# Kernel tuning notes

Measured on AMD Instinct MI355X. Metric: run time of the kernel, lower is better.

Reference implementation:

```python
import jax, jax.numpy as jnp
import numpy as np

D_MODEL = 512
NUM_HEADS = 8
D_K = D_MODEL // NUM_HEADS


def setup_inputs() -> dict:
    key = jax.random.key(0)
    ks = jax.random.split(key, 13)
    B, S = 2, 4096
    s = 1.0 / np.sqrt(D_MODEL)
    inp = {
        'Q': jax.random.normal(ks[0], (B, S, D_MODEL), jnp.float32),
        'K': jax.random.normal(ks[1], (B, S, D_MODEL), jnp.float32),
        'V': jax.random.normal(ks[2], (B, S, D_MODEL), jnp.float32),
        'mask': jax.random.randint(ks[3], (B, S), 0, 2, jnp.int32),
        'W_q': jax.random.normal(ks[4], (D_MODEL, D_MODEL), jnp.float32) * s,
        'b_q': jnp.zeros((D_MODEL,), jnp.float32),
        'W_k': jax.random.normal(ks[5], (D_MODEL, D_MODEL), jnp.float32) * s,
        'b_k': jnp.zeros((D_MODEL,), jnp.float32),
        'W_v': jax.random.normal(ks[6], (D_MODEL, D_MODEL), jnp.float32) * s,
        'b_v': jnp.zeros((D_MODEL,), jnp.float32),
        'W_o': jax.random.normal(ks[7], (D_MODEL, D_MODEL), jnp.float32) * s,
        'b_o': jnp.zeros((D_MODEL,), jnp.float32),
    }
    return inp


def _split_heads(x):
    B, S, _ = x.shape
    return x.reshape(B, S, NUM_HEADS, D_K).transpose(0, 2, 1, 3)  # [B,H,S,d_k]


def reference(Q, K, V, mask, W_q, b_q, W_k, b_k, W_v, b_v, W_o, b_o):
    q = _split_heads(Q @ W_q.T + b_q)
    k = _split_heads(K @ W_k.T + b_k)
    v = _split_heads(V @ W_v.T + b_v)
    scores = jnp.einsum('bhqd,bhkd->bhqk', q, k) / jnp.sqrt(jnp.float32(D_K))
    # mask [B,S] broadcast over heads and query dim (key dim masked)
    scores = jnp.where(mask[:, None, None, :] == 0, jnp.float32(-1e9), scores)
    probs = jax.nn.softmax(scores, axis=-1)
    attn = jnp.einsum('bhqk,bhkd->bhqd', probs, v)
    B, H, S, dk = attn.shape
    combined = attn.transpose(0, 2, 1, 3).reshape(B, S, D_MODEL)
    return combined @ W_o.T + b_o
```

## Files before the change

kernel.cpp:

```cpp
#include <hip/hip_runtime.h>
#include <hip/hip_bf16.h>

typedef _Float16 h8 __attribute__((ext_vector_type(8)));
typedef _Float16 h4 __attribute__((ext_vector_type(4)));
typedef _Float16 h2 __attribute__((ext_vector_type(2)));
typedef float f2 __attribute__((ext_vector_type(2)));
typedef float f4 __attribute__((ext_vector_type(4)));
typedef float f16v __attribute__((ext_vector_type(16)));

#define MFMA32(a, b, c) __builtin_amdgcn_mfma_f32_32x32x16_f16(a, b, c, 0, 0, 0)

static constexpr int DM = 512;
static constexpr int SL = 4096;
static constexpr int NH = 8;
static constexpr int DK = 64;
static constexpr int NB = 2;

__device__ __forceinline__ h2 pk2(float a, float b) {
    return __builtin_bit_cast(h2, __builtin_amdgcn_cvt_pkrtz(a, b));
}
__device__ __forceinline__ h8 cvt8(float4 x, float4 y) {
    union { h2 h[4]; h8 v; } u;
    u.h[0] = pk2(x.x, x.y); u.h[1] = pk2(x.z, x.w);
    u.h[2] = pk2(y.x, y.y); u.h[3] = pk2(y.z, y.w);
    return u.v;
}

__global__ __launch_bounds__(256) void proj_qkv_kernel(
    const float* __restrict__ Qin, const float* __restrict__ Kin,
    const float* __restrict__ Vin,
    const float* __restrict__ Wq, const float* __restrict__ Wk,
    const float* __restrict__ Wv,
    const float* __restrict__ bq, const float* __restrict__ bk,
    const float* __restrict__ bv,
    _Float16* __restrict__ qo, _Float16* __restrict__ ko,
    _Float16* __restrict__ vTo)
{
    const int bid = blockIdx.x;
    const int op  = (bid & 7) * 96 + (bid >> 3);
    const int nt    = op & 3;
    const int panel = op >> 2;
    const int which = panel >> 6;
    const int mt    = panel & 63;

    const float* __restrict__ X    = which == 0 ? Qin : (which == 1 ? Kin : Vin);
    const float* __restrict__ W    = which == 0 ? Wq  : (which == 1 ? Wk  : Wv);
    const float* __restrict__ bias = which == 0 ? bq  : (which == 1 ? bk  : bv);

    __shared__ __align__(16) _Float16 As[2][4096];
    __shared__ __align__(16) _Float16 Bs[2][4096];
    __shared__ __align__(16) _Float16 Vtr[64][144];

    const int t   = threadIdx.x;
    const int w   = t >> 6;
    const int l   = t & 63;
    const int l31 = l & 31;
    const int hi  = l >> 5;
    const int mbase = mt * 128;
    const int nbase = nt * 128;
    const int wm = (w >> 1) * 64;
    const int wn = (w & 1) * 64;

    const int id0 = t, id1 = 256 + t;
    const int r0 = id0 >> 2, c0 = id0 & 3;
    const int r1 = id1 >> 2, c1 = id1 & 3;
    const int sl0 = (c0 ^ (r0 & 3)) * 8;
    const int sl1 = (c1 ^ (r1 & 3)) * 8;
    const float* Xp0 = X + (size_t)(mbase + r0) * DM + c0 * 8;
    const float* Xp1 = X + (size_t)(mbase + r1) * DM + c1 * 8;
    const float* Wp0 = W + (size_t)(nbase + r0) * DM + c0 * 8;
    const float* Wp1 = W + (size_t)(nbase + r1) * DM + c1 * 8;

    f16v acc[2][2] = {};

    {
        float4 a00 = *(const float4*)(Xp0), a01 = *(const float4*)(Xp0 + 4);
        float4 a10 = *(const float4*)(Xp1), a11 = *(const float4*)(Xp1 + 4);
        float4 b00 = *(const float4*)(Wp0), b01 = *(const float4*)(Wp0 + 4);
        float4 b10 = *(const float4*)(Wp1), b11 = *(const float4*)(Wp1 + 4);
        *(h8*)&As[0][r0 * 32 + sl0] = cvt8(a00, a01);
        *(h8*)&As[0][r1 * 32 + sl1] = cvt8(a10, a11);
        *(h8*)&Bs[0][r0 * 32 + sl0] = cvt8(b00, b01);
        *(h8*)&Bs[0][r1 * 32 + sl1] = cvt8(b10, b11);
    }
    __syncthreads();

    int cur = 0;
    for (int step = 0; step < 16; ++step) {
        const int kn = (step + 1) * 32;
        float4 a00, a01, a10, a11, b00, b01, b10, b11;
        const bool more = step + 1 < 16;
        if (more) {
            a00 = *(const float4*)(Xp0 + kn); a01 = *(const float4*)(Xp0 + kn + 4);
            a10 = *(const float4*)(Xp1 + kn); a11 = *(const float4*)(Xp1 + kn + 4);
            b00 = *(const float4*)(Wp0 + kn); b01 = *(const float4*)(Wp0 + kn + 4);
            b10 = *(const float4*)(Wp1 + kn); b11 = *(const float4*)(Wp1 + kn + 4);
        }

        const _Float16* Ac = As[cur];
        const _Float16* Bc = Bs[cur];
        h8 af[2][2], bf[2][2];
#pragma unroll
        for (int ti = 0; ti < 2; ++ti)
#pragma unroll
            for (int s = 0; s < 2; ++s)
                af[ti][s] = *(const h8*)&Ac[(wm + ti * 32 + l31) * 32 +
                                            (((2 * s + hi) ^ (l31 & 3)) << 3)];
#pragma unroll
        for (int tj = 0; tj < 2; ++tj)
#pragma unroll
            for (int s = 0; s < 2; ++s)
                bf[tj][s] = *(const h8*)&Bc[(wn + tj * 32 + l31) * 32 +
                                            (((2 * s + hi) ^ (l31 & 3)) << 3)];
        __builtin_amdgcn_s_setprio(1);
#pragma unroll
        for (int ti = 0; ti < 2; ++ti)
#pragma unroll
            for (int tj = 0; tj < 2; ++tj)
#pragma unroll
                for (int s = 0; s < 2; ++s)
                    acc[ti][tj] = MFMA32(af[ti][s], bf[tj][s], acc[ti][tj]);
        __builtin_amdgcn_s_setprio(0);

        if (more) {
            const int nb2 = cur ^ 1;
            *(h8*)&As[nb2][r0 * 32 + sl0] = cvt8(a00, a01);
            *(h8*)&As[nb2][r1 * 32 + sl1] = cvt8(a10, a11);
            *(h8*)&Bs[nb2][r0 * 32 + sl0] = cvt8(b00, b01);
            *(h8*)&Bs[nb2][r1 * 32 + sl1] = cvt8(b10, b11);
        }
        __syncthreads();
        cur ^= 1;
    }

    if (which < 2) {
        _Float16* dst = (which == 0) ? qo : ko;
#pragma unroll
        for (int tj = 0; tj < 2; ++tj) {
            const int n  = nbase + wn + tj * 32 + l31;
            const float bb = bias[n];
            const int hh = n >> 6;
            const int d  = n & 63;
#pragma unroll
            for (int ti = 0; ti < 2; ++ti) {
#pragma unroll
                for (int j = 0; j < 4; ++j) {
#pragma unroll
                    for (int c = 0; c < 4; ++c) {
                        const int m = mbase + wm + ti * 32 + 8 * j + 4 * hi + c;
                        const int bi = m >> 12;
                        const int s  = m & 4095;
                        dst[((size_t)(bi * NH + hh) * SL + s) * DK + d] =
                            (_Float16)(acc[ti][tj][4 * j + c] + bb);
                    }
                }
            }
        }
    } else {
        const int bi = mbase >> 12;
        const int s0 = mbase & 4095;
#pragma unroll
        for (int nh = 0; nh < 2; ++nh) {
            __syncthreads();
            if ((w & 1) == nh) {
#pragma unroll
                for (int tj = 0; tj < 2; ++tj) {
                    const int d = tj * 32 + l31;
                    const float bb = bias[nbase + nh * 64 + d];
#pragma unroll
                    for (int ti = 0; ti < 2; ++ti) {
#pragma unroll
                        for (int j = 0; j < 4; ++j) {
                            h2 x0 = pk2(acc[ti][tj][4 * j] + bb,
                                        acc[ti][tj][4 * j + 1] + bb);
                            h2 x1 = pk2(acc[ti][tj][4 * j + 2] + bb,
                                        acc[ti][tj][4 * j + 3] + bb);
                            h4 val = {x0[0], x0[1], x1[0], x1[1]};
                            *(h4*)&Vtr[d][wm + ti * 32 + 8 * j + 4 * hi] = val;
                        }
                    }
                }
            }
            __syncthreads();
            {
                const int d = t >> 2, part = t & 3;
                const int hh = nt * 2 + nh;
                _Float16* dstv = vTo + ((size_t)(bi * NH + hh) * DK + d) * SL +
                                 s0 + part * 32;
                h8 v0 = *(const h8*)&Vtr[d][part * 32];
                h8 v1 = *(const h8*)&Vtr[d][part * 32 + 8];
                h8 v2 = *(const h8*)&Vtr[d][part * 32 + 16];
                h8 v3 = *(const h8*)&Vtr[d][part * 32 + 24];
                *(h8*)(dstv)      = v0;
                *(h8*)(dstv + 8)  = v1;
                *(h8*)(dstv + 16) = v2;
                *(h8*)(dstv + 24) = v3;
            }
        }
    }
}

static constexpr int QBLK  = 256;
static constexpr int KSPL  = 2;
static constexpr int KHALF = SL / KSPL;
static constexpr int NTS   = KHALF / 64;

__device__ __forceinline__ void stage_tiles(
    _Float16* Ktb, _Float16* Vtb,
    const _Float16* kbh, const _Float16* vbh, int kb, int t)
{
    const int w = t >> 6;
    const char* ksrc = (const char*)(kbh + (size_t)kb * DK);
    {
        const int c  = t;
        const int kr = c >> 3;
        const int sl = c & 7;
        const int srow = (kr & ~12) | ((kr & 4) << 1) | ((kr & 8) >> 1);
        const int cs = srow * 8 + (sl ^ (kr & 7));
        char* dst = (char*)Ktb + (size_t)w * 1024;
        __builtin_amdgcn_global_load_lds(
            (const __attribute__((address_space(1))) void*)(ksrc + (size_t)cs * 16),
            (__attribute__((address_space(3))) void*)dst, 16, 0, 0);
    }
    {
        const int c  = t;
        const int d  = c >> 3;
        const int cs = (c & 7) ^ (d & 7);
        const _Float16* src = vbh + (size_t)d * SL + kb + cs * 8;
        char* dst = (char*)Vtb + (size_t)w * 1024;
        __builtin_amdgcn_global_load_lds(
            (const __attribute__((address_space(1))) void*)src,
            (__attribute__((address_space(3))) void*)dst, 16, 0, 0);
    }
}

__global__ __launch_bounds__(512, 4) void attn_kernel(
    const _Float16* __restrict__ qg, const _Float16* __restrict__ kg,
    const _Float16* __restrict__ vTg, const int* __restrict__ mask,
    _Float16* __restrict__ o_ws, float* __restrict__ l_ws)
{
    const int t   = threadIdx.x;
    const int w   = t >> 6;
    const int l   = t & 63;
    const int l31 = l & 31;
    const int hi  = l >> 5;
    const int r7  = l31 & 7;
    const int hh  = blockIdx.x & 7;
    const int b   = blockIdx.x >> 3;
    const int qt  = blockIdx.y;
    const int split = blockIdx.z;
    const int koff  = split * KHALF;

    const _Float16* qbh = qg  + (size_t)(b * NH + hh) * SL * DK;
    const _Float16* kbh = kg  + (size_t)(b * NH + hh) * SL * DK;
    const _Float16* vbh = vTg + (size_t)(b * NH + hh) * DK * SL;
    const int* mrow = mask + b * SL;

    __shared__ __align__(16) _Float16 Kt[2][4096];
    __shared__ __align__(16) _Float16 Vt[2][4096];
    __shared__ __align__(16) float bias_tab[KHALF];

    {
        int4 v = *(const int4*)&mrow[koff + t * 4];
        f4 bv;
        bv[0] = v.x ? 0.f : -1e38f; bv[1] = v.y ? 0.f : -1e38f;
        bv[2] = v.z ? 0.f : -1e38f; bv[3] = v.w ? 0.f : -1e38f;
        *(f4*)&bias_tab[t * 4] = bv;
    }

    const _Float16 sch = (_Float16)(0.125f * 1.44269504089f);
    const h8 sc8 = {sch, sch, sch, sch, sch, sch, sch, sch};
    h8 qf[4];
    {
        const _Float16* qp = qbh + (size_t)(qt * QBLK + w * 32 + l31) * DK + hi * 8;
#pragma unroll
        for (int st = 0; st < 4; ++st)
            qf[st] = *(const h8*)(qp + st * 16) * sc8;
    }

    stage_tiles(Kt[0], Vt[0], kbh, vbh, koff, t);
    __syncthreads();

    f16v ov[2] = {};
    float lsum = 0.f;
    const h2 one2 = {(_Float16)1.0f, (_Float16)1.0f};

    int cur = 0;
    for (int kt = 0; kt < NTS; ++kt) {
        const int kb = koff + kt * 64;
        if (kt + 1 < NTS)
            stage_tiles(Kt[cur ^ 1], Vt[cur ^ 1], kbh, vbh, kb + 64, t);

        const _Float16* Kc = Kt[cur];
        const _Float16* Vc = Vt[cur];
        const int lb = kt * 64;

        f16v sc[2];
#pragma unroll
        for (int s = 0; s < 2; ++s) {
            union { f2 q[8]; f16v v; } u;
#pragma unroll
            for (int j = 0; j < 4; ++j) {
                const int base = lb + s * 32 + ((j >> 1) << 4) +
                                 ((j & 1) << 2) + (hi << 3);
                u.q[2 * j]     = *(const f2*)&bias_tab[base];
                u.q[2 * j + 1] = *(const f2*)&bias_tab[base + 2];
            }
            sc[s] = u.v;
        }

        __builtin_amdgcn_s_setprio(1);
#pragma unroll
        for (int s = 0; s < 2; ++s) {
            const int rb = (s * 32 + l31) * 64;
#pragma unroll
            for (int st = 0; st < 4; ++st) {
                h8 a = *(const h8*)&Kc[rb + (((st * 2 + hi) ^ r7) << 3)];
                sc[s] = MFMA32(a, qf[st], sc[s]);
            }
        }
        __builtin_amdgcn_s_setprio(0);

#pragma unroll
        for (int s = 0; s < 2; ++s)
#pragma unroll
            for (int r = 0; r < 16; ++r)
                sc[s][r] = __builtin_amdgcn_exp2f(sc[s][r]);

        __builtin_amdgcn_s_setprio(1);
#pragma unroll
        for (int ks = 0; ks < 4; ++ks) {
            const int s  = ks >> 1;
            const int e0 = (ks & 1) * 8;
            union { h2 h[4]; h8 v; } pf;
#pragma unroll
            for (int u2 = 0; u2 < 4; ++u2) {
                pf.h[u2] = pk2(sc[s][e0 + 2 * u2], sc[s][e0 + 2 * u2 + 1]);
                lsum = __builtin_amdgcn_fdot2(pf.h[u2], one2, lsum, false);
            }
#pragma unroll
            for (int ds = 0; ds < 2; ++ds) {
                h8 av = *(const h8*)&Vc[(ds * 32 + l31) * 64 +
                                        (((ks * 2 + hi) ^ r7) << 3)];
                ov[ds] = MFMA32(av, pf.v, ov[ds]);
            }
        }
        __builtin_amdgcn_s_setprio(0);

        __syncthreads();
        cur ^= 1;
    }

    lsum += __shfl_xor(lsum, 32);
    const int qrow = qt * QBLK + w * 32 + l31;
    if (hi == 0)
        l_ws[((size_t)(split * NB + b) * SL + qrow) * NH + hh] = lsum * 0x1p-12f;

    const float osc = 0x1p-12f;
    _Float16* orow = o_ws + ((size_t)split * NB * SL + (size_t)b * SL + qrow) * DM +
                     hh * DK;
#pragma unroll
    for (int ds = 0; ds < 2; ++ds) {
#pragma unroll
        for (int j = 0; j < 4; ++j) {
            const int d0 = ds * 32 + j * 8 + hi * 4;
            h2 w0 = pk2(ov[ds][4 * j] * osc,     ov[ds][4 * j + 1] * osc);
            h2 w1 = pk2(ov[ds][4 * j + 2] * osc, ov[ds][4 * j + 3] * osc);
            h4 val = {w0[0], w0[1], w1[0], w1[1]};
            *(h4*)&orow[d0] = val;
        }
    }
}

__global__ __launch_bounds__(256) void out_proj_kernel(
    const _Float16* __restrict__ o_ws, const float* __restrict__ l_ws,
    const float* __restrict__ Wo, const float* __restrict__ bo,
    float* __restrict__ out)
{
    const int bid = blockIdx.x;
    const int op  = (bid & 7) * 64 + (bid >> 3);
    const int nt  = op & 3;
    const int mt  = op >> 2;

    __shared__ __align__(16) _Float16 As[2][2048];
    __shared__ __align__(16) _Float16 Bs[2][4096];
    __shared__ float Linv[64][8];

    const int t   = threadIdx.x;
    const int w   = t >> 6;
    const int l   = t & 63;
    const int l31 = l & 31;
    const int hi  = l >> 5;
    const int mbase = mt * 64;
    const int nbase = nt * 128;

    const size_t NSL = (size_t)NB * SL;

#pragma unroll
    for (int e = 0; e < 2; ++e) {
        const int idx = t * 2 + e;
        const int r = idx >> 3, h = idx & 7;
        const int m = mbase + r;
        const int bb = m >> 12;
        const int qr = m & 4095;
        float s = 0.f;
#pragma unroll
        for (int sp = 0; sp < KSPL; ++sp)
            s += l_ws[((size_t)(sp * NB + bb) * SL + qr) * NH + h];
        Linv[r][h] = 1.0f / s;
    }

    const int ar = t >> 2, ac = t & 3;
    const int asl = (ac ^ (ar & 3)) * 8;
    const _Float16* Ap = o_ws + (size_t)(mbase + ar) * DM + ac * 8;

    const int id0 = t, id1 = 256 + t;
    const int r0 = id0 >> 2, c0 = id0 & 3;
    const int r1 = id1 >> 2, c1 = id1 & 3;
    const int sl0 = (c0 ^ (r0 & 3)) * 8;
    const int sl1 = (c1 ^ (r1 & 3)) * 8;
    const float* Wp0 = Wo + (size_t)(nbase + r0) * DM + c0 * 8;
    const float* Wp1 = Wo + (size_t)(nbase + r1) * DM + c1 * 8;

    __syncthreads();

    auto combine = [&](int kk) -> h8 {
        h8 x0 = *(const h8*)(Ap + kk);
        h8 x1 = *(const h8*)(Ap + kk + NSL * DM);
        const float li = Linv[ar][((kk + ac * 8) >> 6) & 7];
        union { h2 h[4]; h8 v; } u;
#pragma unroll
        for (int e = 0; e < 4; ++e) {
            float a0 = ((float)x0[2 * e]     + (float)x1[2 * e])     * li;
            float a1 = ((float)x0[2 * e + 1] + (float)x1[2 * e + 1]) * li;
            u.h[e] = pk2(a0, a1);
        }
        return u.v;
    };

    f16v acc[2] = {};

    {
        *(h8*)&As[0][ar * 32 + asl] = combine(0);
        float4 b00 = *(const float4*)(Wp0), b01 = *(const float4*)(Wp0 + 4);
        float4 b10 = *(const float4*)(Wp1), b11 = *(const float4*)(Wp1 + 4);
        *(h8*)&Bs[0][r0 * 32 + sl0] = cvt8(b00, b01);
        *(h8*)&Bs[0][r1 * 32 + sl1] = cvt8(b10, b11);
    }
    __syncthreads();

    int cur = 0;
    for (int step = 0; step < 16; ++step) {
        const int kn = (step + 1) * 32;
        const bool more = step + 1 < 16;
        h8 av;
        float4 b00, b01, b10, b11;
        if (more) {
            av  = combine(kn);
            b00 = *(const float4*)(Wp0 + kn); b01 = *(const float4*)(Wp0 + kn + 4);
            b10 = *(const float4*)(Wp1 + kn); b11 = *(const float4*)(Wp1 + kn + 4);
        }

        const _Float16* Ac = As[cur];
        const _Float16* Bc = Bs[cur];
        h8 af[2][2], bf[2];
#pragma unroll
        for (int ti = 0; ti < 2; ++ti)
#pragma unroll
            for (int s = 0; s < 2; ++s)
                af[ti][s] = *(const h8*)&Ac[(ti * 32 + l31) * 32 +
                                            (((2 * s + hi) ^ (l31 & 3)) << 3)];
#pragma unroll
        for (int s = 0; s < 2; ++s)
            bf[s] = *(const h8*)&Bc[(w * 32 + l31) * 32 +
                                    (((2 * s + hi) ^ (l31 & 3)) << 3)];
        __builtin_amdgcn_s_setprio(1);
#pragma unroll
        for (int ti = 0; ti < 2; ++ti)
#pragma unroll
            for (int s = 0; s < 2; ++s)
                acc[ti] = MFMA32(af[ti][s], bf[s], acc[ti]);
        __builtin_amdgcn_s_setprio(0);

        if (more) {
            const int nb2 = cur ^ 1;
            *(h8*)&As[nb2][ar * 32 + asl] = av;
            *(h8*)&Bs[nb2][r0 * 32 + sl0] = cvt8(b00, b01);
            *(h8*)&Bs[nb2][r1 * 32 + sl1] = cvt8(b10, b11);
        }
        __syncthreads();
        cur ^= 1;
    }

    const int n = nbase + w * 32 + l31;
    const float bb = bo[n];
#pragma unroll
    for (int ti = 0; ti < 2; ++ti) {
#pragma unroll
        for (int j = 0; j < 4; ++j) {
#pragma unroll
            for (int c = 0; c < 4; ++c) {
                const int m = mbase + ti * 32 + 8 * j + 4 * hi + c;
                out[(size_t)m * DM + n] = acc[ti][4 * j + c] + bb;
            }
        }
    }
}

extern "C" void kernel_launch(void* const* d_in, const int* in_sizes, int n_in,
                              void* d_out, int out_size, void* d_ws, size_t ws_size,
                              hipStream_t stream)
{
    const float* Q    = (const float*)d_in[0];
    const float* K    = (const float*)d_in[1];
    const float* V    = (const float*)d_in[2];
    const int*   mask = (const int*)d_in[3];
    const float* Wq   = (const float*)d_in[4];
    const float* bq   = (const float*)d_in[5];
    const float* Wk   = (const float*)d_in[6];
    const float* bk   = (const float*)d_in[7];
    const float* Wv   = (const float*)d_in[8];
    const float* bv   = (const float*)d_in[9];
    const float* Wo   = (const float*)d_in[10];
    const float* bo   = (const float*)d_in[11];
    float* out = (float*)d_out;

    _Float16* ws = (_Float16*)d_ws;
    const size_t per = (size_t)NB * NH * SL * DK;
    _Float16* q_ws  = ws;
    _Float16* k_ws  = ws + per;
    _Float16* vT_ws = ws + 2 * per;
    _Float16* o_ws  = ws + 3 * per;
    float*    l_ws  = (float*)(ws + 3 * per + KSPL * per);

    proj_qkv_kernel<<<dim3(768), 256, 0, stream>>>(
        Q, K, V, Wq, Wk, Wv, bq, bk, bv, q_ws, k_ws, vT_ws);

    attn_kernel<<<dim3(NB * NH, SL / QBLK, KSPL), 512, 0, stream>>>(
        q_ws, k_ws, vT_ws, mask, o_ws, l_ws);

    out_proj_kernel<<<dim3(512), 256, 0, stream>>>(o_ws, l_ws, Wo, bo, out);
}
```

Baseline: 125.3 us.

## Software-pipeline QK^T of next tile with softmax/PV of current tile

After: 139.9 us. 11.7% more time.

```diff
diff --git a/kernel.cpp b/kernel.cpp
--- a/kernel.cpp
+++ b/kernel.cpp
@@ -205,36 +205,37 @@
 static constexpr int KHALF = SL / KSPL;
 static constexpr int NTS   = KHALF / 64;
 
-__device__ __forceinline__ void stage_tiles(
-    _Float16* Ktb, _Float16* Vtb,
-    const _Float16* kbh, const _Float16* vbh, int kb, int t)
+__device__ __forceinline__ void stage_k(
+    _Float16* Ktb, const _Float16* kbh, int kb, int t)
 {
     const int w = t >> 6;
     const char* ksrc = (const char*)(kbh + (size_t)kb * DK);
-    {
-        const int c  = t;
-        const int kr = c >> 3;
-        const int sl = c & 7;
-        const int srow = (kr & ~12) | ((kr & 4) << 1) | ((kr & 8) >> 1);
-        const int cs = srow * 8 + (sl ^ (kr & 7));
-        char* dst = (char*)Ktb + (size_t)w * 1024;
-        __builtin_amdgcn_global_load_lds(
-            (const __attribute__((address_space(1))) void*)(ksrc + (size_t)cs * 16),
-            (__attribute__((address_space(3))) void*)dst, 16, 0, 0);
-    }
-    {
-        const int c  = t;
-        const int d  = c >> 3;
-        const int cs = (c & 7) ^ (d & 7);
-        const _Float16* src = vbh + (size_t)d * SL + kb + cs * 8;
-        char* dst = (char*)Vtb + (size_t)w * 1024;
-        __builtin_amdgcn_global_load_lds(
-            (const __attribute__((address_space(1))) void*)src,
-            (__attribute__((address_space(3))) void*)dst, 16, 0, 0);
-    }
-}
-
-__global__ __launch_bounds__(512, 4) void attn_kernel(
+    const int c  = t;
+    const int kr = c >> 3;
+    const int sl = c & 7;
+    const int srow = (kr & ~12) | ((kr & 4) << 1) | ((kr & 8) >> 1);
+    const int cs = srow * 8 + (sl ^ (kr & 7));
+    char* dst = (char*)Ktb + (size_t)w * 1024;
+    __builtin_amdgcn_global_load_lds(
+        (const __attribute__((address_space(1))) void*)(ksrc + (size_t)cs * 16),
+        (__attribute__((address_space(3))) void*)dst, 16, 0, 0);
+}
+
+__device__ __forceinline__ void stage_v(
+    _Float16* Vtb, const _Float16* vbh, int kb, int t)
+{
+    const int w = t >> 6;
+    const int c  = t;
+    const int d  = c >> 3;
+    const int cs = (c & 7) ^ (d & 7);
+    const _Float16* src = vbh + (size_t)d * SL + kb + cs * 8;
+    char* dst = (char*)Vtb + (size_t)w * 1024;
+    __builtin_amdgcn_global_load_lds(
+        (const __attribute__((address_space(1))) void*)src,
+        (__attribute__((address_space(3))) void*)dst, 16, 0, 0);
+}
+
+__global__ __launch_bounds__(512, 2) void attn_kernel(
     const _Float16* __restrict__ qg, const _Float16* __restrict__ kg,
     const _Float16* __restrict__ vTg, const int* __restrict__ mask,
     _Float16* __restrict__ o_ws, float* __restrict__ l_ws)
@@ -257,7 +258,7 @@
     const int* mrow = mask + b * SL;
 
     __shared__ __align__(16) _Float16 Kt[2][4096];
-    __shared__ __align__(16) _Float16 Vt[2][4096];
+    __shared__ __align__(16) _Float16 Vt[3][4096];
     __shared__ __align__(16) float bias_tab[KHALF];
 
     {
@@ -278,64 +279,72 @@
             qf[st] = *(const h8*)(qp + st * 16) * sc8;
     }
 
-    stage_tiles(Kt[0], Vt[0], kbh, vbh, koff, t);
+    stage_k(Kt[0], kbh, koff, t);
+    stage_v(Vt[0], vbh, koff, t);
+    stage_k(Kt[1], kbh, koff + 64, t);
+    stage_v(Vt[1], vbh, koff + 64, t);
+    __syncthreads();
+
+    auto QK = [&](const _Float16* Kc, int lb, f16v (&o)[2]) {
+        f16v s[2];
+#pragma unroll
+        for (int si = 0; si < 2; ++si) {
+            union { f2 q[8]; f16v v; } u;
+#pragma unroll
+            for (int j = 0; j < 4; ++j) {
+                const int base = lb + si * 32 + ((j >> 1) << 4) +
+                                 ((j & 1) << 2) + (hi << 3);
+                u.q[2 * j]     = *(const f2*)&bias_tab[base];
+                u.q[2 * j + 1] = *(const f2*)&bias_tab[base + 2];
+            }
+            s[si] = u.v;
+        }
+        __builtin_amdgcn_s_setprio(1);
+#pragma unroll
+        for (int si = 0; si < 2; ++si) {
+            const int rb = (si * 32 + l31) * 64;
+#pragma unroll
+            for (int st = 0; st < 4; ++st) {
+                h8 a = *(const h8*)&Kc[rb + (((st * 2 + hi) ^ r7) << 3)];
+                s[si] = MFMA32(a, qf[st], s[si]);
+            }
+        }
+        __builtin_amdgcn_s_setprio(0);
+        o[0] = s[0]; o[1] = s[1];
+    };
+
+    f16v scA[2], scB[2];
+    QK(&Kt[0][0], 0, scA);
     __syncthreads();
 
     f16v ov[2] = {};
     float lsum = 0.f;
     const h2 one2 = {(_Float16)1.0f, (_Float16)1.0f};
 
-    int cur = 0;
-    for (int kt = 0; kt < NTS; ++kt) {
-        const int kb = koff + kt * 64;
-        if (kt + 1 < NTS)
-            stage_tiles(Kt[cur ^ 1], Vt[cur ^ 1], kbh, vbh, kb + 64, t);
-
-        const _Float16* Kc = Kt[cur];
-        const _Float16* Vc = Vt[cur];
-        const int lb = kt * 64;
-
-        f16v sc[2];
-#pragma unroll
-        for (int s = 0; s < 2; ++s) {
-            union { f2 q[8]; f16v v; } u;
-#pragma unroll
-            for (int j = 0; j < 4; ++j) {
-                const int base = lb + s * 32 + ((j >> 1) << 4) +
-                                 ((j & 1) << 2) + (hi << 3);
-                u.q[2 * j]     = *(const f2*)&bias_tab[base];
-                u.q[2 * j + 1] = *(const f2*)&bias_tab[base + 2];
-            }
-            sc[s] = u.v;
-        }
-
+    for (int tt = 0; tt < NTS; ++tt) {
+        if (tt + 2 < NTS) {
+            stage_k(Kt[tt & 1], kbh, koff + (tt + 2) * 64, t);
+            stage_v(Vt[(tt + 2) % 3], vbh, koff + (tt + 2) * 64, t);
+        }
+        if (tt + 1 < NTS)
+            QK(&Kt[(tt + 1) & 1][0], (tt + 1) * 64, scB);
+
+#pragma unroll
+        for (int si = 0; si < 2; ++si)
+#pragma unroll
+            for (int r = 0; r < 16; ++r)
+                scA[si][r] = __builtin_amdgcn_exp2f(scA[si][r]);
+
+        const _Float16* Vc = &Vt[tt % 3][0];
         __builtin_amdgcn_s_setprio(1);
 #pragma unroll
-        for (int s = 0; s < 2; ++s) {
-            const int rb = (s * 32 + l31) * 64;
-#pragma unroll
-            for (int st = 0; st < 4; ++st) {
-                h8 a = *(const h8*)&Kc[rb + (((st * 2 + hi) ^ r7) << 3)];
-                sc[s] = MFMA32(a, qf[st], sc[s]);
-            }
-        }
-        __builtin_amdgcn_s_setprio(0);
-
-#pragma unroll
-        for (int s = 0; s < 2; ++s)
-#pragma unroll
-            for (int r = 0; r < 16; ++r)
-                sc[s][r] = __builtin_amdgcn_exp2f(sc[s][r]);
-
-        __builtin_amdgcn_s_setprio(1);
-#pragma unroll
         for (int ks = 0; ks < 4; ++ks) {
-            const int s  = ks >> 1;
+            const int si = ks >> 1;
             const int e0 = (ks & 1) * 8;
             union { h2 h[4]; h8 v; } pf;
 #pragma unroll
             for (int u2 = 0; u2 < 4; ++u2) {
-                pf.h[u2] = pk2(sc[s][e0 + 2 * u2], sc[s][e0 + 2 * u2 + 1]);
+                pf.h[u2] = pk2(scA[si][e0 + 2 * u2], scA[si][e0 + 2 * u2 + 1]);
                 lsum = __builtin_amdgcn_fdot2(pf.h[u2], one2, lsum, false);
             }
 #pragma unroll
@@ -348,7 +357,8 @@
         __builtin_amdgcn_s_setprio(0);
 
         __syncthreads();
-        cur ^= 1;
+        scA[0] = scB[0];
+        scA[1] = scB[1];
     }
 
     lsum += __shfl_xor(lsum, 32);
```

## Process two query groups per wave in attention to reuse K/V LDS reads

Applied to the files above, without the earlier changes.

Result: faster. 122.0 us (median of 2 runs) (-2.6%).

```diff
diff --git a/kernel.cpp b/kernel.cpp
--- a/kernel.cpp
+++ b/kernel.cpp
@@ -211,30 +211,32 @@
 {
     const int w = t >> 6;
     const char* ksrc = (const char*)(kbh + (size_t)kb * DK);
-    {
-        const int c  = t;
+#pragma unroll
+    for (int p = 0; p < 2; ++p) {
+        const int c  = p * 256 + t;
         const int kr = c >> 3;
         const int sl = c & 7;
         const int srow = (kr & ~12) | ((kr & 4) << 1) | ((kr & 8) >> 1);
         const int cs = srow * 8 + (sl ^ (kr & 7));
-        char* dst = (char*)Ktb + (size_t)w * 1024;
+        char* dst = (char*)Ktb + (size_t)(p * 256 + w * 64) * 16;
         __builtin_amdgcn_global_load_lds(
             (const __attribute__((address_space(1))) void*)(ksrc + (size_t)cs * 16),
             (__attribute__((address_space(3))) void*)dst, 16, 0, 0);
     }
-    {
-        const int c  = t;
+#pragma unroll
+    for (int p = 0; p < 2; ++p) {
+        const int c  = p * 256 + t;
         const int d  = c >> 3;
         const int cs = (c & 7) ^ (d & 7);
         const _Float16* src = vbh + (size_t)d * SL + kb + cs * 8;
-        char* dst = (char*)Vtb + (size_t)w * 1024;
+        char* dst = (char*)Vtb + (size_t)(p * 256 + w * 64) * 16;
         __builtin_amdgcn_global_load_lds(
             (const __attribute__((address_space(1))) void*)src,
             (__attribute__((address_space(3))) void*)dst, 16, 0, 0);
     }
 }
 
-__global__ __launch_bounds__(512, 4) void attn_kernel(
+__global__ __launch_bounds__(256, 2) void attn_kernel(
     const _Float16* __restrict__ qg, const _Float16* __restrict__ kg,
     const _Float16* __restrict__ vTg, const int* __restrict__ mask,
     _Float16* __restrict__ o_ws, float* __restrict__ l_ws)
@@ -260,29 +262,32 @@
     __shared__ __align__(16) _Float16 Vt[2][4096];
     __shared__ __align__(16) float bias_tab[KHALF];
 
-    {
-        int4 v = *(const int4*)&mrow[koff + t * 4];
+#pragma unroll
+    for (int j = 0; j < 2; ++j) {
+        int4 v = *(const int4*)&mrow[koff + t * 8 + j * 4];
         f4 bv;
         bv[0] = v.x ? 0.f : -1e38f; bv[1] = v.y ? 0.f : -1e38f;
         bv[2] = v.z ? 0.f : -1e38f; bv[3] = v.w ? 0.f : -1e38f;
-        *(f4*)&bias_tab[t * 4] = bv;
+        *(f4*)&bias_tab[t * 8 + j * 4] = bv;
     }
 
     const _Float16 sch = (_Float16)(0.125f * 1.44269504089f);
     const h8 sc8 = {sch, sch, sch, sch, sch, sch, sch, sch};
-    h8 qf[4];
-    {
-        const _Float16* qp = qbh + (size_t)(qt * QBLK + w * 32 + l31) * DK + hi * 8;
+    h8 qf[2][4];
+#pragma unroll
+    for (int qgp = 0; qgp < 2; ++qgp) {
+        const _Float16* qp = qbh +
+            (size_t)(qt * QBLK + w * 64 + qgp * 32 + l31) * DK + hi * 8;
 #pragma unroll
         for (int st = 0; st < 4; ++st)
-            qf[st] = *(const h8*)(qp + st * 16) * sc8;
+            qf[qgp][st] = *(const h8*)(qp + st * 16) * sc8;
     }
 
     stage_tiles(Kt[0], Vt[0], kbh, vbh, koff, t);
     __syncthreads();
 
-    f16v ov[2] = {};
-    float lsum = 0.f;
+    f16v ov[2][2] = {};
+    float lsum0 = 0.f, lsum1 = 0.f;
     const h2 one2 = {(_Float16)1.0f, (_Float16)1.0f};
 
     int cur = 0;
@@ -295,54 +300,61 @@
         const _Float16* Vc = Vt[cur];
         const int lb = kt * 64;
 
-        f16v sc[2];
-#pragma unroll
-        for (int s = 0; s < 2; ++s) {
+        f16v sc[2][2];
+#pragma unroll
+        for (int kgp = 0; kgp < 2; ++kgp) {
             union { f2 q[8]; f16v v; } u;
 #pragma unroll
             for (int j = 0; j < 4; ++j) {
-                const int base = lb + s * 32 + ((j >> 1) << 4) +
+                const int base = lb + kgp * 32 + ((j >> 1) << 4) +
                                  ((j & 1) << 2) + (hi << 3);
                 u.q[2 * j]     = *(const f2*)&bias_tab[base];
                 u.q[2 * j + 1] = *(const f2*)&bias_tab[base + 2];
             }
-            sc[s] = u.v;
+            sc[kgp][0] = u.v;
+            sc[kgp][1] = u.v;
         }
 
         __builtin_amdgcn_s_setprio(1);
 #pragma unroll
-        for (int s = 0; s < 2; ++s) {
-            const int rb = (s * 32 + l31) * 64;
+        for (int kgp = 0; kgp < 2; ++kgp) {
+            const int rb = (kgp * 32 + l31) * 64;
 #pragma unroll
             for (int st = 0; st < 4; ++st) {
                 h8 a = *(const h8*)&Kc[rb + (((st * 2 + hi) ^ r7) << 3)];
-                sc[s] = MFMA32(a, qf[st], sc[s]);
+                sc[kgp][0] = MFMA32(a, qf[0][st], sc[kgp][0]);
+                sc[kgp][1] = MFMA32(a, qf[1][st], sc[kgp][1]);
             }
         }
         __builtin_amdgcn_s_setprio(0);
 
 #pragma unroll
-        for (int s = 0; s < 2; ++s)
-#pragma unroll
-            for (int r = 0; r < 16; ++r)
-                sc[s][r] = __builtin_amdgcn_exp2f(sc[s][r]);
+        for (int kgp = 0; kgp < 2; ++kgp)
+#pragma unroll
+            for (int qgp = 0; qgp < 2; ++qgp)
+#pragma unroll
+                for (int r = 0; r < 16; ++r)
+                    sc[kgp][qgp][r] = __builtin_amdgcn_exp2f(sc[kgp][qgp][r]);
 
         __builtin_amdgcn_s_setprio(1);
 #pragma unroll
         for (int ks = 0; ks < 4; ++ks) {
-            const int s  = ks >> 1;
-            const int e0 = (ks & 1) * 8;
-            union { h2 h[4]; h8 v; } pf;
+            const int kgp = ks >> 1;
+            const int e0  = (ks & 1) * 8;
+            union { h2 h[4]; h8 v; } pf0, pf1;
 #pragma unroll
             for (int u2 = 0; u2 < 4; ++u2) {
-                pf.h[u2] = pk2(sc[s][e0 + 2 * u2], sc[s][e0 + 2 * u2 + 1]);
-                lsum = __builtin_amdgcn_fdot2(pf.h[u2], one2, lsum, false);
+                pf0.h[u2] = pk2(sc[kgp][0][e0 + 2 * u2], sc[kgp][0][e0 + 2 * u2 + 1]);
+                lsum0 = __builtin_amdgcn_fdot2(pf0.h[u2], one2, lsum0, false);
+                pf1.h[u2] = pk2(sc[kgp][1][e0 + 2 * u2], sc[kgp][1][e0 + 2 * u2 + 1]);
+                lsum1 = __builtin_amdgcn_fdot2(pf1.h[u2], one2, lsum1, false);
             }
 #pragma unroll
             for (int ds = 0; ds < 2; ++ds) {
                 h8 av = *(const h8*)&Vc[(ds * 32 + l31) * 64 +
                                         (((ks * 2 + hi) ^ r7) << 3)];
-                ov[ds] = MFMA32(av, pf.v, ov[ds]);
+                ov[ds][0] = MFMA32(av, pf0.v, ov[ds][0]);
+                ov[ds][1] = MFMA32(av, pf1.v, ov[ds][1]);
             }
         }
         __builtin_amdgcn_s_setprio(0);
@@ -351,23 +363,27 @@
         cur ^= 1;
     }
 
-    lsum += __shfl_xor(lsum, 32);
-    const int qrow = qt * QBLK + w * 32 + l31;
-    if (hi == 0)
-        l_ws[((size_t)(split * NB + b) * SL + qrow) * NH + hh] = lsum * 0x1p-12f;
-
     const float osc = 0x1p-12f;
-    _Float16* orow = o_ws + ((size_t)split * NB * SL + (size_t)b * SL + qrow) * DM +
-                     hh * DK;
-#pragma unroll
-    for (int ds = 0; ds < 2; ++ds) {
-#pragma unroll
-        for (int j = 0; j < 4; ++j) {
-            const int d0 = ds * 32 + j * 8 + hi * 4;
-            h2 w0 = pk2(ov[ds][4 * j] * osc,     ov[ds][4 * j + 1] * osc);
-            h2 w1 = pk2(ov[ds][4 * j + 2] * osc, ov[ds][4 * j + 3] * osc);
-            h4 val = {w0[0], w0[1], w1[0], w1[1]};
-            *(h4*)&orow[d0] = val;
+#pragma unroll
+    for (int qgp = 0; qgp < 2; ++qgp) {
+        float ls = qgp ? lsum1 : lsum0;
+        ls += __shfl_xor(ls, 32);
+        const int qrow = qt * QBLK + w * 64 + qgp * 32 + l31;
+        if (hi == 0)
+            l_ws[((size_t)(split * NB + b) * SL + qrow) * NH + hh] = ls * 0x1p-12f;
+
+        _Float16* orow = o_ws +
+            ((size_t)split * NB * SL + (size_t)b * SL + qrow) * DM + hh * DK;
+#pragma unroll
+        for (int ds = 0; ds < 2; ++ds) {
+#pragma unroll
+            for (int j = 0; j < 4; ++j) {
+                const int d0 = ds * 32 + j * 8 + hi * 4;
+                h2 w0 = pk2(ov[ds][qgp][4 * j] * osc,     ov[ds][qgp][4 * j + 1] * osc);
+                h2 w1 = pk2(ov[ds][qgp][4 * j + 2] * osc, ov[ds][qgp][4 * j + 3] * osc);
+                h4 val = {w0[0], w0[1], w1[0], w1[1]};
+                *(h4*)&orow[d0] = val;
+            }
         }
     }
 }
@@ -536,7 +552,7 @@
     proj_qkv_kernel<<<dim3(768), 256, 0, stream>>>(
         Q, K, V, Wq, Wk, Wv, bq, bk, bv, q_ws, k_ws, vT_ws);
 
-    attn_kernel<<<dim3(NB * NH, SL / QBLK, KSPL), 512, 0, stream>>>(
+    attn_kernel<<<dim3(NB * NH, SL / QBLK, KSPL), 256, 0, stream>>>(
         q_ws, k_ws, vT_ws, mask, o_ws, l_ws);
 
     out_proj_kernel<<<dim3(512), 256, 0, stream>>>(o_ws, l_ws, Wo, bo, out);
```
